# Optimization experiments

Hardware: AMD Instinct MI355X
Metric: run time of the kernel (lower is better)

Reference implementation:

```python
import jax, jax.numpy as jnp
import numpy as np

N_NODES = 100000
N_EDGES = 1600000
D = 64
N_TARGETS = 100
N_GRAPHS = 512


def gcn_conv(x, W, b, src, dst):
    """GCNConv with default add_self_loops=True, symmetric normalization."""
    n = x.shape[0]
    h = x @ W  # [N, out]
    ones = jnp.ones(dst.shape[0], dtype=h.dtype)
    deg = jax.ops.segment_sum(ones, dst, num_segments=n) + 1.0  # +1 for self-loop
    dinv = jax.lax.rsqrt(deg)
    norm = dinv[src] * dinv[dst]  # [E]
    agg = jax.ops.segment_sum(h[src] * norm[:, None], dst, num_segments=n)
    agg = agg + h * (dinv * dinv)[:, None]  # self-loop contribution: 1/deg[i] * h[i]
    return agg + b


def setup_inputs() -> dict:
    key = jax.random.key(0)
    ks = jax.random.split(key, 12)
    x = jax.random.normal(ks[0], (N_NODES, D), dtype=jnp.float32)
    edge_index = jax.random.randint(ks[1], (2, N_EDGES), 0, N_NODES, dtype=jnp.int64)
    batch_seg = jnp.sort(jax.random.randint(ks[2], (N_NODES,), 0, N_GRAPHS, dtype=jnp.int64))
    s = 1.0 / np.sqrt(D)
    W1 = jax.random.normal(ks[3], (D, D), dtype=jnp.float32) * s
    b1 = jnp.zeros((D,), dtype=jnp.float32)
    W2 = jax.random.normal(ks[4], (D, D), dtype=jnp.float32) * s
    b2 = jnp.zeros((D,), dtype=jnp.float32)
    W3 = jax.random.normal(ks[5], (D, D), dtype=jnp.float32) * s
    b3 = jnp.zeros((D,), dtype=jnp.float32)
    Wout = jax.random.normal(ks[6], (D, N_TARGETS), dtype=jnp.float32) * s
    bout = jnp.zeros((N_TARGETS,), dtype=jnp.float32)
    return {"x": x, "W1": W1, "b1": b1, "W2": W2, "b2": b2, "W3": W3, "b3": b3,
            "Wout": Wout, "bout": bout, "edge_index": edge_index, "batch_seg": batch_seg}


def reference(x, W1, b1, W2, b2, W3, b3, Wout, bout, edge_index, batch_seg):
    src, dst = edge_index[0], edge_index[1]
    h = jax.nn.relu(gcn_conv(x, W1, b1, src, dst))   # dropout p=0 -> identity
    h = jax.nn.relu(gcn_conv(h, W2, b2, src, dst))
    h = gcn_conv(h, W3, b3, src, dst)
    counts = jax.ops.segment_sum(jnp.ones(h.shape[0], h.dtype), batch_seg, num_segments=N_GRAPHS)
    pooled = jax.ops.segment_sum(h, batch_seg, num_segments=N_GRAPHS) / jnp.maximum(counts, 1.0)[:, None]
    return pooled @ Wout + bout  # [N_GRAPHS, N_TARGETS]
```

## Files before the change

### kernel.cpp

```cpp
#include <hip/hip_runtime.h>

#define N_NODES   100000
#define N_EDGES   1600000
#define D         64
#define N_TARGETS 100
#define N_GRAPHS  512
#define NBUCK     391
#define EPB       4096
#define BCAP      6144
#define MM_NPW    16

typedef _Float16 half4 __attribute__((ext_vector_type(4)));
typedef _Float16 half8 __attribute__((ext_vector_type(8)));
typedef __fp16   hf2   __attribute__((ext_vector_type(2)));
typedef __fp16   hf8   __attribute__((ext_vector_type(8)));

#if defined(__has_builtin)
#if __has_builtin(__builtin_amdgcn_fdot2)
#define USE_DOT2 1
#endif
#endif

__global__ void k_init(int* __restrict__ gcur, float* __restrict__ poolz) {
    int i = blockIdx.x * blockDim.x + threadIdx.x;
    if (i < NBUCK) gcur[i] = 0;
    if (i < N_GRAPHS * D + N_GRAPHS) poolz[i] = 0.0f;
}

__global__ void k_prepW(const float* __restrict__ W, _Float16* __restrict__ out) {
    int t = threadIdx.x;
#pragma unroll
    for (int it = 0; it < 2; ++it) {
        int idx = t + it * 256;
        int m = idx >> 3, c = idx & 7;
        half8 hv;
#pragma unroll
        for (int tt = 0; tt < 8; ++tt)
            hv[tt] = (_Float16)W[(8 * c + tt) * 64 + m];
        *(half8*)&out[m * 64 + ((c ^ (m & 7)) * 8)] = hv;
    }
}

__global__ void __launch_bounds__(256)
k_binA(const int* __restrict__ src, const int* __restrict__ dst,
       int* __restrict__ gcur, unsigned long long* __restrict__ staged) {
    __shared__ int hist[NBUCK];
    __shared__ int boff[NBUCK];
    int tid = threadIdx.x;
    for (int i = tid; i < NBUCK; i += 256) hist[i] = 0;
    __syncthreads();

    int e0 = blockIdx.x * EPB;
    int s_[16], d_[16], r_[16];
#pragma unroll
    for (int k = 0; k < 16; ++k) {
        int e = e0 + k * 256 + tid;
        if (e < N_EDGES) {
            s_[k] = src[e];
            d_[k] = dst[e];
            r_[k] = atomicAdd(&hist[d_[k] >> 8], 1);
        } else {
            d_[k] = -1;
        }
    }
    __syncthreads();
    for (int b = tid; b < NBUCK; b += 256) {
        int h = hist[b];
        boff[b] = (h > 0) ? atomicAdd(&gcur[b], h) : 0;
    }
    __syncthreads();
#pragma unroll
    for (int k = 0; k < 16; ++k) {
        if (d_[k] >= 0) {
            int b = d_[k] >> 8;
            staged[(size_t)b * BCAP + boff[b] + r_[k]] =
                ((unsigned long long)(unsigned)d_[k] << 32) | (unsigned)s_[k];
        }
    }
}

__global__ void k_scanB(const int* __restrict__ gcur, int* __restrict__ bstart) {
    __shared__ int s[512];
    int t = threadIdx.x;
    int v = (t < NBUCK) ? gcur[t] : 0;
    s[t] = v;
    __syncthreads();
    for (int off = 1; off < 512; off <<= 1) {
        int x = (t >= off) ? s[t - off] : 0;
        __syncthreads();
        s[t] += x;
        __syncthreads();
    }
    if (t < NBUCK) bstart[t] = s[t] - v;
    if (t == 0) bstart[NBUCK] = N_EDGES;
}

__global__ void __launch_bounds__(256)
k_binB(const unsigned long long* __restrict__ staged, const int* __restrict__ gcur,
       const int* __restrict__ bstart, int* __restrict__ esrc,
       int* __restrict__ base, float* __restrict__ dinv) {
    __shared__ int s[256];
    __shared__ int lbase[256];
    __shared__ int cur[256];
    int b = blockIdx.x;
    int t = threadIdx.x;
    int n0 = b << 8;
    int Eb = gcur[b];
    int Sb = bstart[b];
    const unsigned long long* sl = staged + (size_t)b * BCAP;

    cur[t] = 0;
    __syncthreads();
    for (int k = t; k < Eb; k += 256) {
        int dl = ((int)(sl[k] >> 32)) & 255;
        atomicAdd(&cur[dl], 1);
    }
    __syncthreads();
    int v = cur[t];
    s[t] = v;
    __syncthreads();
    for (int off = 1; off < 256; off <<= 1) {
        int x = (t >= off) ? s[t - off] : 0;
        __syncthreads();
        s[t] += x;
        __syncthreads();
    }
    lbase[t] = s[t] - v;
    int gi = n0 + t;
    if (gi < N_NODES) {
        base[gi] = Sb + (s[t] - v);
        dinv[gi] = rsqrtf((float)v + 1.0f);
    }
    if (b == 0 && t == 0) base[N_NODES] = N_EDGES;
    cur[t] = 0;
    __syncthreads();
    for (int k = t; k < Eb; k += 256) {
        unsigned long long pd = sl[k];
        int dl = ((int)(pd >> 32)) & 255;
        int pos = Sb + lbase[dl] + atomicAdd(&cur[dl], 1);
        esrc[pos] = (int)(pd & 0xffffffffu);
    }
}

__global__ void __launch_bounds__(256)
k_mm(const float* __restrict__ X, const float* __restrict__ W,
     const float* __restrict__ dinv, _Float16* __restrict__ Y16) {
    __shared__ float W1L[D * D];
    __shared__ float aSh[4][D];
    int tid = threadIdx.x;
#pragma unroll
    for (int it = 0; it < 4; ++it) {
        int idx = (tid + it * 256) * 4;
        *(float4*)&W1L[idx] = *(const float4*)(W + idx);
    }
    __syncthreads();

    int wv = tid >> 6, lane = tid & 63;
    float wreg[D];
#pragma unroll
    for (int k = 0; k < D; ++k)
        wreg[k] = W1L[k * D + lane];

    int i0 = (blockIdx.x * 4 + wv) * MM_NPW;
    if (i0 >= N_NODES) return;
    int iEnd = i0 + MM_NPW; if (iEnd > N_NODES) iEnd = N_NODES;

    float xv = X[(size_t)i0 * D + lane];
    for (int i = i0; i < iEnd; ++i) {
        int inext = (i + 1 < N_NODES) ? (i + 1) : i;
        float xnext = X[(size_t)inext * D + lane];

        aSh[wv][lane] = xv;
        asm volatile("s_waitcnt lgkmcnt(0)" ::: "memory");

        float ac0 = 0.f, ac1 = 0.f, ac2 = 0.f, ac3 = 0.f;
#pragma unroll
        for (int c = 0; c < 16; ++c) {
            float4 a4 = *(const float4*)&aSh[wv][c * 4];
            ac0 = fmaf(a4.x, wreg[4 * c + 0], ac0);
            ac1 = fmaf(a4.y, wreg[4 * c + 1], ac1);
            ac2 = fmaf(a4.z, wreg[4 * c + 2], ac2);
            ac3 = fmaf(a4.w, wreg[4 * c + 3], ac3);
        }
        float acc = (ac0 + ac1) + (ac2 + ac3);
        Y16[(size_t)i * D + lane] = (_Float16)(acc * dinv[i]);
        xv = xnext;
    }
}

__global__ void __launch_bounds__(256)
k_pullmm(const _Float16* __restrict__ H, const int* __restrict__ esrc,
         const int* __restrict__ base, const float* __restrict__ dinv,
         const float* __restrict__ b_in, const _Float16* __restrict__ Whg,
         _Float16* __restrict__ Hout) {
    __shared__ _Float16 WhL[D * D];
    __shared__ _Float16 aSh[4][D];
    {
#pragma unroll
        for (int it = 0; it < 2; ++it) {
            int t = threadIdx.x + it * 256;
            *(half8*)&WhL[t * 8] = *(const half8*)&Whg[t * 8];
        }
    }
    __syncthreads();

    int wv   = threadIdx.x >> 6;
    int lane = threadIdx.x & 63;
    int i    = blockIdx.x * 4 + wv;
    int s0 = base[i], s1 = base[i + 1];

    float a0 = (float)H[(size_t)i * D + lane];
    float a1 = 0.f, a2 = 0.f, a3 = 0.f;

    int p = s0;
    while (p < s1) {
        int cnt = s1 - p;
        if (cnt > 64) cnt = 64;
        int ed = (lane < cnt) ? esrc[p + lane] : 0;
        int j = 0;
        for (; j + 4 <= cnt; j += 4) {
            int e0 = __builtin_amdgcn_readlane(ed, j);
            int e1 = __builtin_amdgcn_readlane(ed, j + 1);
            int e2 = __builtin_amdgcn_readlane(ed, j + 2);
            int e3 = __builtin_amdgcn_readlane(ed, j + 3);
            _Float16 h0 = H[(size_t)e0 * D + lane];
            _Float16 h1 = H[(size_t)e1 * D + lane];
            _Float16 h2 = H[(size_t)e2 * D + lane];
            _Float16 h3 = H[(size_t)e3 * D + lane];
            a0 += (float)h0; a1 += (float)h1; a2 += (float)h2; a3 += (float)h3;
        }
        for (; j < cnt; ++j) {
            int e0 = __builtin_amdgcn_readlane(ed, j);
            a0 += (float)H[(size_t)e0 * D + lane];
        }
        p += cnt;
    }
    float agg = (a0 + a1) + (a2 + a3);

    float di = dinv[i];
    float av = fmaxf(fmaf(agg, di, b_in[lane]), 0.f);
    aSh[wv][lane] = (_Float16)av;
    asm volatile("s_waitcnt lgkmcnt(0)" ::: "memory");

    float part = 0.f;
#pragma unroll
    for (int c = 0; c < 8; ++c) {
        hf8 a8 = *(const hf8*)&aSh[wv][c * 8];
        hf8 w8 = *(const hf8*)&WhL[lane * 64 + ((c ^ (lane & 7)) * 8)];
#ifdef USE_DOT2
#pragma unroll
        for (int q = 0; q < 4; ++q) {
            hf2 ap; ap.x = a8[2 * q]; ap.y = a8[2 * q + 1];
            hf2 wp; wp.x = w8[2 * q]; wp.y = w8[2 * q + 1];
            part = __builtin_amdgcn_fdot2(ap, wp, part, false);
        }
#else
#pragma unroll
        for (int t = 0; t < 8; ++t)
            part = fmaf((float)a8[t], (float)w8[t], part);
#endif
    }
    Hout[(size_t)i * D + lane] = (_Float16)(part * di);
}

__global__ void __launch_bounds__(256)
k_pull(const _Float16* __restrict__ H, const int* __restrict__ esrc,
       const int* __restrict__ base, const float* __restrict__ dinv,
       const float* __restrict__ b, _Float16* __restrict__ AGG16) {
    int wv   = threadIdx.x >> 6;
    int lane = threadIdx.x & 63;
    int i    = blockIdx.x * 4 + wv;
    int s0 = base[i], s1 = base[i + 1];

    float a0 = (float)H[(size_t)i * D + lane];
    float a1 = 0.f, a2 = 0.f, a3 = 0.f;

    int p = s0;
    while (p < s1) {
        int cnt = s1 - p;
        if (cnt > 64) cnt = 64;
        int ed = (lane < cnt) ? esrc[p + lane] : 0;
        int j = 0;
        for (; j + 4 <= cnt; j += 4) {
            int e0 = __builtin_amdgcn_readlane(ed, j);
            int e1 = __builtin_amdgcn_readlane(ed, j + 1);
            int e2 = __builtin_amdgcn_readlane(ed, j + 2);
            int e3 = __builtin_amdgcn_readlane(ed, j + 3);
            _Float16 h0 = H[(size_t)e0 * D + lane];
            _Float16 h1 = H[(size_t)e1 * D + lane];
            _Float16 h2 = H[(size_t)e2 * D + lane];
            _Float16 h3 = H[(size_t)e3 * D + lane];
            a0 += (float)h0; a1 += (float)h1; a2 += (float)h2; a3 += (float)h3;
        }
        for (; j < cnt; ++j) {
            int e0 = __builtin_amdgcn_readlane(ed, j);
            a0 += (float)H[(size_t)e0 * D + lane];
        }
        p += cnt;
    }
    float agg = (a0 + a1) + (a2 + a3);
    float di = dinv[i];
    AGG16[(size_t)i * D + lane] = (_Float16)fmaf(agg, di, b[lane]);
}

__global__ void __launch_bounds__(256)
k_pool_seg(const _Float16* __restrict__ H16, const int* __restrict__ seg,
           float* __restrict__ pooled, float* __restrict__ counts) {
    int wave = threadIdx.x >> 6;
    int lane = threadIdx.x & 63;
    int n0 = (blockIdx.x * 4 + wave) * 64;
    if (n0 >= N_NODES) return;
    int nEnd = n0 + 64;
    if (nEnd > N_NODES) nEnd = N_NODES;
    int cur = seg[n0];
    float acc = 0.0f;
    int run = 0;
    for (int n = n0; n < nEnd; ++n) {
        int gsg = seg[n];
        if (gsg != cur) {
            atomicAdd(&pooled[(size_t)cur * D + lane], acc);
            if (lane == 0) atomicAdd(&counts[cur], (float)run);
            acc = 0.0f; run = 0;
            cur = gsg;
        }
        acc += (float)H16[(size_t)n * D + lane];
        run += 1;
    }
    atomicAdd(&pooled[(size_t)cur * D + lane], acc);
    if (lane == 0) atomicAdd(&counts[cur], (float)run);
}

__global__ void k_out(const float* __restrict__ pooled, const float* __restrict__ counts,
                      const float* __restrict__ Wout, const float* __restrict__ bout,
                      float* __restrict__ out) {
    __shared__ float prow[D];
    int g = blockIdx.x;
    int t = threadIdx.x;
    if (t < D) prow[t] = pooled[(size_t)g * D + t] / fmaxf(counts[g], 1.0f);
    __syncthreads();
    if (t < N_TARGETS) {
        float acc = bout[t];
#pragma unroll
        for (int k = 0; k < D; ++k)
            acc = fmaf(prow[k], Wout[k * N_TARGETS + t], acc);
        out[g * N_TARGETS + t] = acc;
    }
}


extern "C" void kernel_launch(void* const* d_in, const int* in_sizes, int n_in,
                              void* d_out, int out_size, void* d_ws, size_t ws_size,
                              hipStream_t stream) {
    const float* x    = (const float*)d_in[0];
    const float* W1   = (const float*)d_in[1];
    const float* b1   = (const float*)d_in[2];
    const float* W2   = (const float*)d_in[3];
    const float* b2   = (const float*)d_in[4];
    const float* W3   = (const float*)d_in[5];
    const float* b3   = (const float*)d_in[6];
    const float* Wout = (const float*)d_in[7];
    const float* bout = (const float*)d_in[8];
    const int*   eidx = (const int*)d_in[9];
    const int*   seg  = (const int*)d_in[10];
    const int* src = eidx;
    const int* dst = eidx + N_EDGES;
    float* out = (float*)d_out;

    _Float16* H16A   = (_Float16*)d_ws;
    _Float16* H16B   = H16A + (size_t)N_NODES * D;
    _Float16* AGG16  = H16B;
    unsigned long long* staged = (unsigned long long*)d_ws;
    int*      esrc   = (int*)(H16B + (size_t)N_NODES * D);
    float*    dinv   = (float*)(esrc + N_EDGES);
    int*      base   = (int*)(dinv + N_NODES);
    float*    pooled = (float*)(base + N_NODES + 4);
    float*    counts = pooled + N_GRAPHS * D;
    int*      gcur   = (int*)(counts + N_GRAPHS);
    int*      bstart = gcur + 512;
    _Float16* WhA    = (_Float16*)(bstart + 512);
    _Float16* WhB    = WhA + 4096;

    const int NB = (N_NODES + 255) / 256;

    k_prepW<<<1, 256, 0, stream>>>(W2, WhA);
    k_prepW<<<1, 256, 0, stream>>>(W3, WhB);

    k_init<<<130, 256, 0, stream>>>(gcur, pooled);
    k_binA<<<(N_EDGES + EPB - 1) / EPB, 256, 0, stream>>>(src, dst, gcur, staged);
    k_scanB<<<1, 512, 0, stream>>>(gcur, bstart);
    k_binB<<<NBUCK, 256, 0, stream>>>(staged, gcur, bstart, esrc, base, dinv);

    const int MMB = (N_NODES + 4 * MM_NPW - 1) / (4 * MM_NPW);
    k_mm<<<MMB, 256, 0, stream>>>(x, W1, dinv, H16A);
    k_pullmm<<<N_NODES / 4, 256, 0, stream>>>(H16A, esrc, base, dinv, b1, WhA, H16B);
    k_pullmm<<<N_NODES / 4, 256, 0, stream>>>(H16B, esrc, base, dinv, b2, WhB, H16A);
    k_pull<<<N_NODES / 4, 256, 0, stream>>>(H16A, esrc, base, dinv, b3, AGG16);

    k_pool_seg<<<NB, 256, 0, stream>>>(AGG16, seg, pooled, counts);
    k_out<<<N_GRAPHS, 128, 0, stream>>>(pooled, counts, Wout, bout, out);
}
```

Baseline: 357.1 us.

## Gather neighbor rows with 16-byte loads across eight lane groups

The pull kernels are restructured so each wavefront handles eight edges at once. Each group of 8 lanes loads a full 128-byte fp16 row with half8 vector loads, and a cross-group shuffle-xor reduction combines the partial sums at the end. This replaces the old scheme of one 2-byte load per lane per edge, cutting the number of load instructions and increasing memory-level parallelism in the gather. In exchange it adds shuffle overhead, keeps 8 accumulator registers per lane, and does part of the summation in fp16 (v0+v1), which slightly changes numerical rounding.

```diff
diff --git a/kernel.cpp b/kernel.cpp
--- a/kernel.cpp
+++ b/kernel.cpp
@@ -206,11 +206,16 @@
 
     int wv   = threadIdx.x >> 6;
     int lane = threadIdx.x & 63;
+    int g = lane >> 3, l = lane & 7;
     int i    = blockIdx.x * 4 + wv;
     int s0 = base[i], s1 = base[i + 1];
 
-    float a0 = (float)H[(size_t)i * D + lane];
-    float a1 = 0.f, a2 = 0.f, a3 = 0.f;
+    float acc[8] = {0.f, 0.f, 0.f, 0.f, 0.f, 0.f, 0.f, 0.f};
+    if (g == 0) {
+        half8 sv = *(const half8*)(H + (size_t)i * D + l * 8);
+#pragma unroll
+        for (int q = 0; q < 8; ++q) acc[q] = (float)sv[q];
+    }
 
     int p = s0;
     while (p < s1) {
@@ -218,28 +223,60 @@
         if (cnt > 64) cnt = 64;
         int ed = (lane < cnt) ? esrc[p + lane] : 0;
         int j = 0;
-        for (; j + 4 <= cnt; j += 4) {
-            int e0 = __builtin_amdgcn_readlane(ed, j);
-            int e1 = __builtin_amdgcn_readlane(ed, j + 1);
-            int e2 = __builtin_amdgcn_readlane(ed, j + 2);
-            int e3 = __builtin_amdgcn_readlane(ed, j + 3);
-            _Float16 h0 = H[(size_t)e0 * D + lane];
-            _Float16 h1 = H[(size_t)e1 * D + lane];
-            _Float16 h2 = H[(size_t)e2 * D + lane];
-            _Float16 h3 = H[(size_t)e3 * D + lane];
-            a0 += (float)h0; a1 += (float)h1; a2 += (float)h2; a3 += (float)h3;
-        }
-        for (; j < cnt; ++j) {
-            int e0 = __builtin_amdgcn_readlane(ed, j);
-            a0 += (float)H[(size_t)e0 * D + lane];
+        for (; j + 32 <= cnt; j += 32) {
+            int e0 = __shfl(ed, j + g, 64);
+            int e1 = __shfl(ed, j + 8 + g, 64);
+            int e2 = __shfl(ed, j + 16 + g, 64);
+            int e3 = __shfl(ed, j + 24 + g, 64);
+            half8 v0 = *(const half8*)(H + (size_t)(unsigned)e0 * D + l * 8);
+            half8 v1 = *(const half8*)(H + (size_t)(unsigned)e1 * D + l * 8);
+            half8 v2 = *(const half8*)(H + (size_t)(unsigned)e2 * D + l * 8);
+            half8 v3 = *(const half8*)(H + (size_t)(unsigned)e3 * D + l * 8);
+            half8 s01 = v0 + v1;
+            half8 s23 = v2 + v3;
+#pragma unroll
+            for (int q = 0; q < 8; ++q)
+                acc[q] += (float)s01[q] + (float)s23[q];
+        }
+        for (; j + 8 <= cnt; j += 8) {
+            int e0 = __shfl(ed, j + g, 64);
+            half8 v0 = *(const half8*)(H + (size_t)(unsigned)e0 * D + l * 8);
+#pragma unroll
+            for (int q = 0; q < 8; ++q) acc[q] += (float)v0[q];
+        }
+        if (j < cnt) {
+            int idx = j + g;
+            int e0 = __shfl(ed, idx & 63, 64);
+            if (idx < cnt) {
+                half8 v0 = *(const half8*)(H + (size_t)(unsigned)e0 * D + l * 8);
+#pragma unroll
+                for (int q = 0; q < 8; ++q) acc[q] += (float)v0[q];
+            }
         }
         p += cnt;
     }
-    float agg = (a0 + a1) + (a2 + a3);
+#pragma unroll
+    for (int off = 8; off <= 32; off <<= 1) {
+#pragma unroll
+        for (int q = 0; q < 8; ++q)
+            acc[q] += __shfl_xor(acc[q], off, 64);
+    }
 
     float di = dinv[i];
-    float av = fmaxf(fmaf(agg, di, b_in[lane]), 0.f);
-    aSh[wv][lane] = (_Float16)av;
+    if (g == 0) {
+        float4 bl0 = *(const float4*)(b_in + l * 8);
+        float4 bl1 = *(const float4*)(b_in + l * 8 + 4);
+        half8 av;
+        av[0] = (_Float16)fmaxf(fmaf(acc[0], di, bl0.x), 0.f);
+        av[1] = (_Float16)fmaxf(fmaf(acc[1], di, bl0.y), 0.f);
+        av[2] = (_Float16)fmaxf(fmaf(acc[2], di, bl0.z), 0.f);
+        av[3] = (_Float16)fmaxf(fmaf(acc[3], di, bl0.w), 0.f);
+        av[4] = (_Float16)fmaxf(fmaf(acc[4], di, bl1.x), 0.f);
+        av[5] = (_Float16)fmaxf(fmaf(acc[5], di, bl1.y), 0.f);
+        av[6] = (_Float16)fmaxf(fmaf(acc[6], di, bl1.z), 0.f);
+        av[7] = (_Float16)fmaxf(fmaf(acc[7], di, bl1.w), 0.f);
+        *(half8*)&aSh[wv][l * 8] = av;
+    }
     asm volatile("s_waitcnt lgkmcnt(0)" ::: "memory");
 
     float part = 0.f;
@@ -269,11 +306,16 @@
        const float* __restrict__ b, _Float16* __restrict__ AGG16) {
     int wv   = threadIdx.x >> 6;
     int lane = threadIdx.x & 63;
+    int g = lane >> 3, l = lane & 7;
     int i    = blockIdx.x * 4 + wv;
     int s0 = base[i], s1 = base[i + 1];
 
-    float a0 = (float)H[(size_t)i * D + lane];
-    float a1 = 0.f, a2 = 0.f, a3 = 0.f;
+    float acc[8] = {0.f, 0.f, 0.f, 0.f, 0.f, 0.f, 0.f, 0.f};
+    if (g == 0) {
+        half8 sv = *(const half8*)(H + (size_t)i * D + l * 8);
+#pragma unroll
+        for (int q = 0; q < 8; ++q) acc[q] = (float)sv[q];
+    }
 
     int p = s0;
     while (p < s1) {
@@ -281,26 +323,60 @@
         if (cnt > 64) cnt = 64;
         int ed = (lane < cnt) ? esrc[p + lane] : 0;
         int j = 0;
-        for (; j + 4 <= cnt; j += 4) {
-            int e0 = __builtin_amdgcn_readlane(ed, j);
-            int e1 = __builtin_amdgcn_readlane(ed, j + 1);
-            int e2 = __builtin_amdgcn_readlane(ed, j + 2);
-            int e3 = __builtin_amdgcn_readlane(ed, j + 3);
-            _Float16 h0 = H[(size_t)e0 * D + lane];
-            _Float16 h1 = H[(size_t)e1 * D + lane];
-            _Float16 h2 = H[(size_t)e2 * D + lane];
-            _Float16 h3 = H[(size_t)e3 * D + lane];
-            a0 += (float)h0; a1 += (float)h1; a2 += (float)h2; a3 += (float)h3;
-        }
-        for (; j < cnt; ++j) {
-            int e0 = __builtin_amdgcn_readlane(ed, j);
-            a0 += (float)H[(size_t)e0 * D + lane];
+        for (; j + 32 <= cnt; j += 32) {
+            int e0 = __shfl(ed, j + g, 64);
+            int e1 = __shfl(ed, j + 8 + g, 64);
+            int e2 = __shfl(ed, j + 16 + g, 64);
+            int e3 = __shfl(ed, j + 24 + g, 64);
+            half8 v0 = *(const half8*)(H + (size_t)(unsigned)e0 * D + l * 8);
+            half8 v1 = *(const half8*)(H + (size_t)(unsigned)e1 * D + l * 8);
+            half8 v2 = *(const half8*)(H + (size_t)(unsigned)e2 * D + l * 8);
+            half8 v3 = *(const half8*)(H + (size_t)(unsigned)e3 * D + l * 8);
+            half8 s01 = v0 + v1;
+            half8 s23 = v2 + v3;
+#pragma unroll
+            for (int q = 0; q < 8; ++q)
+                acc[q] += (float)s01[q] + (float)s23[q];
+        }
+        for (; j + 8 <= cnt; j += 8) {
+            int e0 = __shfl(ed, j + g, 64);
+            half8 v0 = *(const half8*)(H + (size_t)(unsigned)e0 * D + l * 8);
+#pragma unroll
+            for (int q = 0; q < 8; ++q) acc[q] += (float)v0[q];
+        }
+        if (j < cnt) {
+            int idx = j + g;
+            int e0 = __shfl(ed, idx & 63, 64);
+            if (idx < cnt) {
+                half8 v0 = *(const half8*)(H + (size_t)(unsigned)e0 * D + l * 8);
+#pragma unroll
+                for (int q = 0; q < 8; ++q) acc[q] += (float)v0[q];
+            }
         }
         p += cnt;
     }
-    float agg = (a0 + a1) + (a2 + a3);
-    float di = dinv[i];
-    AGG16[(size_t)i * D + lane] = (_Float16)fmaf(agg, di, b[lane]);
+#pragma unroll
+    for (int off = 8; off <= 32; off <<= 1) {
+#pragma unroll
+        for (int q = 0; q < 8; ++q)
+            acc[q] += __shfl_xor(acc[q], off, 64);
+    }
+
+    if (g == 0) {
+        float di = dinv[i];
+        float4 bl0 = *(const float4*)(b + l * 8);
+        float4 bl1 = *(const float4*)(b + l * 8 + 4);
+        half8 o;
+        o[0] = (_Float16)fmaf(acc[0], di, bl0.x);
+        o[1] = (_Float16)fmaf(acc[1], di, bl0.y);
+        o[2] = (_Float16)fmaf(acc[2], di, bl0.z);
+        o[3] = (_Float16)fmaf(acc[3], di, bl0.w);
+        o[4] = (_Float16)fmaf(acc[4], di, bl1.x);
+        o[5] = (_Float16)fmaf(acc[5], di, bl1.y);
+        o[6] = (_Float16)fmaf(acc[6], di, bl1.z);
+        o[7] = (_Float16)fmaf(acc[7], di, bl1.w);
+        *(half8*)(AGG16 + (size_t)i * D + l * 8) = o;
+    }
 }
 
 __global__ void __launch_bounds__(256)
```

New measurement: 347.1 us. 2.8% less time.
